# Kernel optimization log

Hardware: AMD Instinct MI355X
Metric: run time of the kernel (lower is better)

Reference implementation:

```python
import jax, jax.numpy as jnp
import numpy as np

GRID = 14    # grid_size[0]
PATCH = 16   # patch_size[0]

def setup_inputs() -> dict:
    key = jax.random.key(0)
    x = jax.random.normal(key, (32, 96, 224, 224), dtype=jnp.float32)
    return {"x": x}

def reference(x):
    # x: [B, C, H, W] with H = W = GRID*PATCH
    B, C, H, W = x.shape
    g, p = GRID, PATCH
    # [B, C, gi, pi, gj, pj]
    t = x.reshape(B, C, g, p, g, p)
    # L2 norm over (C, gi, gj) for each intra-patch offset (pi, pj) -> [B, p, p]
    sq = jnp.sum(t * t, axis=(1, 2, 4))
    norms = jnp.sqrt(sq)
    # argmax over flattened (pi, pj), pj fastest -> matches torch reshape order
    idx = jnp.argmax(norms.reshape(B, p * p), axis=1)
    si = idx // p  # row shift
    sj = idx % p   # col shift
    # circular pad + translate-by-(si,sj) + crop == circular roll by (-si, -sj)
    out = jax.vmap(lambda xi, a, b: jnp.roll(xi, (-a, -b), axis=(1, 2)))(x, si, sj)
    return out
```

## Files before the change

### kernel.cpp

```cpp
#include <hip/hip_runtime.h>

#define H 224
#define W 224
#define B 32
#define C 96


__global__ void zero_norms_kernel(float* __restrict__ nbuf) {
    int i = blockIdx.x * blockDim.x + threadIdx.x;
    nbuf[i] = 0.0f;
}

template<int DIRECT>
__global__ void norms_kernel(const float* __restrict__ x, float* __restrict__ nbuf) {
    int pi    = blockIdx.x >> 2;
    int slice = blockIdx.x & 3;
    int b     = blockIdx.y;
    int wave  = threadIdx.x >> 6;
    int lane  = threadIdx.x & 63;

    __shared__ float bins[16];
    if (threadIdx.x < 16) bins[threadIdx.x] = 0.0f;
    __syncthreads();

    if (lane < 56) {
        const float* base = x + (size_t)b * C * H * W;
        int c  = slice * 24;
        int gi = wave;
        float a0=0.f,a1=0.f,a2=0.f,a3=0.f;
        float b0=0.f,b1=0.f,b2=0.f,b3=0.f;
        #pragma unroll 2
        for (int it = 0; it < 42; ++it) {
            const float4* rowA = (const float4*)(base + ((size_t)c * H + gi * 16 + pi) * W);
            const float4* rowB = rowA + (size_t)12 * H * W / 4;
            float4 va = rowA[lane];
            float4 vb = rowB[lane];
            a0 += va.x * va.x; a1 += va.y * va.y; a2 += va.z * va.z; a3 += va.w * va.w;
            b0 += vb.x * vb.x; b1 += vb.y * vb.y; b2 += vb.z * vb.z; b3 += vb.w * vb.w;
            gi += 4; if (gi >= 14) { gi -= 14; c += 1; }
        }
        a0 += b0; a1 += b1; a2 += b2; a3 += b3;
        int bse = (lane & 3) << 2;
        atomicAdd(&bins[bse + 0], a0);
        atomicAdd(&bins[bse + 1], a1);
        atomicAdd(&bins[bse + 2], a2);
        atomicAdd(&bins[bse + 3], a3);
    }
    __syncthreads();
    if (threadIdx.x < 16) {
        if (DIRECT)
            nbuf[((slice * B + b) * 16 + pi) * 16 + threadIdx.x] = bins[threadIdx.x];
        else
            atomicAdd(&nbuf[(b * 16 + pi) * 16 + threadIdx.x], bins[threadIdx.x]);
    }
}

template<int DIRECT>
__global__ void argmax_kernel(const float* __restrict__ nbuf, int2* __restrict__ shifts) {
    int b = blockIdx.x;
    int t = threadIdx.x;
    float v = -1.0f;
    int idx = 0;
    for (int r = 0; r < 4; ++r) {
        int i = r * 64 + t;
        float u;
        if (DIRECT) {
            int o = b * 256 + i;
            u = nbuf[o] + nbuf[8192 + o] + nbuf[16384 + o] + nbuf[24576 + o];
        } else {
            u = nbuf[b * 256 + i];
        }
        if (u > v) { v = u; idx = i; }
    }
    for (int off = 32; off > 0; off >>= 1) {
        float ov = __shfl_down(v, off);
        int   oi = __shfl_down(idx, off);
        if (ov > v || (ov == v && oi < idx)) { v = ov; idx = oi; }
    }
    if (t == 0) shifts[b] = make_int2(idx >> 4, idx & 15);
}

template<int R>
__device__ __forceinline__ void roll_body(const float* __restrict__ xb,
                                          float* __restrict__ ob,
                                          int c0, int h0, int sh0,
                                          int q, int lane) {
    int v = lane + q;  if (v >= 56) v -= 56;
    int nl = lane + 1; if (nl >= 56) nl = 0;
    int sh = sh0;
    #pragma unroll
    for (int it = 0; it < 8; ++it) {
        int h = h0 + it * 4;
        const float4* srow = (const float4*)(xb + ((size_t)c0 * H + sh) * W);
        float4*       drow = (float4*)      (ob + ((size_t)c0 * H + h)  * W);
        float4 a = srow[v];
        float4 o;
        if (R == 0) {
            o = a;
        } else {
            float nx = __shfl(a.x, nl);
            float ny = (R >= 2) ? __shfl(a.y, nl) : 0.0f;
            float nz = (R == 3) ? __shfl(a.z, nl) : 0.0f;
            if (R == 1) { o.x = a.y; o.y = a.z; o.z = a.w; o.w = nx; }
            if (R == 2) { o.x = a.z; o.y = a.w; o.z = nx;  o.w = ny; }
            if (R == 3) { o.x = a.w; o.y = nx;  o.z = ny;  o.w = nz; }
        }
        drow[lane] = o;
        sh += 4; if (sh >= H) sh -= H;
    }
}

__global__ void roll_kernel(const float* __restrict__ x, float* __restrict__ out,
                            const int2* __restrict__ shifts) {
    int b     = blockIdx.y;
    int chunk = blockIdx.x;
    int wave  = threadIdx.x >> 6;
    int lane  = threadIdx.x & 63;
    if (lane >= 56) return;

    int2 s = shifts[b];
    int si = s.x, sj = s.y;
    int q = sj >> 2, r = sj & 3;

    int c0 = chunk / 7;
    int h0 = (chunk % 7) * 32 + wave;
    int sh0 = h0 + si; if (sh0 >= H) sh0 -= H;

    const float* xb = x   + (size_t)b * C * H * W;
    float*       ob = out + (size_t)b * C * H * W;

    switch (r) {
        case 0: roll_body<0>(xb, ob, c0, h0, sh0, q, lane); break;
        case 1: roll_body<1>(xb, ob, c0, h0, sh0, q, lane); break;
        case 2: roll_body<2>(xb, ob, c0, h0, sh0, q, lane); break;
        default: roll_body<3>(xb, ob, c0, h0, sh0, q, lane); break;
    }
}

extern "C" void kernel_launch(void* const* d_in, const int* in_sizes, int n_in,
                              void* d_out, int out_size, void* d_ws, size_t ws_size,
                              hipStream_t stream) {
    const float* x = (const float*)d_in[0];
    float* outp = (float*)d_out;

    const size_t directBytes = (size_t)4 * B * 256 * sizeof(float);
    if (ws_size >= directBytes + 256) {
        float* nbuf  = (float*)d_ws;
        int2* shifts = (int2*)((char*)d_ws + directBytes);
        norms_kernel<1><<<dim3(64, 32), 256, 0, stream>>>(x, nbuf);
        argmax_kernel<1><<<32, 64, 0, stream>>>(nbuf, shifts);
        roll_kernel<<<dim3(672, 32), 256, 0, stream>>>(x, outp, shifts);
    } else {
        float* nbuf  = (float*)d_ws;
        int2* shifts = (int2*)((char*)d_ws + 8192 * sizeof(float));
        zero_norms_kernel<<<32, 256, 0, stream>>>(nbuf);
        norms_kernel<0><<<dim3(64, 32), 256, 0, stream>>>(x, nbuf);
        argmax_kernel<0><<<32, 64, 0, stream>>>(nbuf, shifts);
        roll_kernel<<<dim3(672, 32), 256, 0, stream>>>(x, outp, shifts);
    }
}
```

Baseline: 353.2 us.

## Pipeline norms and roll across batch groups in a single fused kernel

Replaces the separate norms, argmax and roll kernels with one fused kernel launched in 17 stages. Each launch computes norms for batch group i and rolls batch group i-1, with the argmax folded into every roll block. The goal is to overlap the reduction pass of one group with the copy pass of the previous group, and to drop the standalone argmax launch. The cost is 17 smaller launches, plus every roll block redoing the argmax reduction. It also assumes the workspace always holds the 4-slice norm buffer and drops the small-workspace fallback.

```diff
diff --git a/kernel.cpp b/kernel.cpp
--- a/kernel.cpp
+++ b/kernel.cpp
@@ -6,79 +6,6 @@
 #define C 96
 
 
-__global__ void zero_norms_kernel(float* __restrict__ nbuf) {
-    int i = blockIdx.x * blockDim.x + threadIdx.x;
-    nbuf[i] = 0.0f;
-}
-
-template<int DIRECT>
-__global__ void norms_kernel(const float* __restrict__ x, float* __restrict__ nbuf) {
-    int pi    = blockIdx.x >> 2;
-    int slice = blockIdx.x & 3;
-    int b     = blockIdx.y;
-    int wave  = threadIdx.x >> 6;
-    int lane  = threadIdx.x & 63;
-
-    __shared__ float bins[16];
-    if (threadIdx.x < 16) bins[threadIdx.x] = 0.0f;
-    __syncthreads();
-
-    if (lane < 56) {
-        const float* base = x + (size_t)b * C * H * W;
-        int c  = slice * 24;
-        int gi = wave;
-        float a0=0.f,a1=0.f,a2=0.f,a3=0.f;
-        float b0=0.f,b1=0.f,b2=0.f,b3=0.f;
-        #pragma unroll 2
-        for (int it = 0; it < 42; ++it) {
-            const float4* rowA = (const float4*)(base + ((size_t)c * H + gi * 16 + pi) * W);
-            const float4* rowB = rowA + (size_t)12 * H * W / 4;
-            float4 va = rowA[lane];
-            float4 vb = rowB[lane];
-            a0 += va.x * va.x; a1 += va.y * va.y; a2 += va.z * va.z; a3 += va.w * va.w;
-            b0 += vb.x * vb.x; b1 += vb.y * vb.y; b2 += vb.z * vb.z; b3 += vb.w * vb.w;
-            gi += 4; if (gi >= 14) { gi -= 14; c += 1; }
-        }
-        a0 += b0; a1 += b1; a2 += b2; a3 += b3;
-        int bse = (lane & 3) << 2;
-        atomicAdd(&bins[bse + 0], a0);
-        atomicAdd(&bins[bse + 1], a1);
-        atomicAdd(&bins[bse + 2], a2);
-        atomicAdd(&bins[bse + 3], a3);
-    }
-    __syncthreads();
-    if (threadIdx.x < 16) {
-        if (DIRECT)
-            nbuf[((slice * B + b) * 16 + pi) * 16 + threadIdx.x] = bins[threadIdx.x];
-        else
-            atomicAdd(&nbuf[(b * 16 + pi) * 16 + threadIdx.x], bins[threadIdx.x]);
-    }
-}
-
-template<int DIRECT>
-__global__ void argmax_kernel(const float* __restrict__ nbuf, int2* __restrict__ shifts) {
-    int b = blockIdx.x;
-    int t = threadIdx.x;
-    float v = -1.0f;
-    int idx = 0;
-    for (int r = 0; r < 4; ++r) {
-        int i = r * 64 + t;
-        float u;
-        if (DIRECT) {
-            int o = b * 256 + i;
-            u = nbuf[o] + nbuf[8192 + o] + nbuf[16384 + o] + nbuf[24576 + o];
-        } else {
-            u = nbuf[b * 256 + i];
-        }
-        if (u > v) { v = u; idx = i; }
-    }
-    for (int off = 32; off > 0; off >>= 1) {
-        float ov = __shfl_down(v, off);
-        int   oi = __shfl_down(idx, off);
-        if (ov > v || (ov == v && oi < idx)) { v = ov; idx = oi; }
-    }
-    if (t == 0) shifts[b] = make_int2(idx >> 4, idx & 15);
-}
 
 template<int R>
 __device__ __forceinline__ void roll_body(const float* __restrict__ xb,
@@ -110,30 +37,91 @@
     }
 }
 
-__global__ void roll_kernel(const float* __restrict__ x, float* __restrict__ out,
-                            const int2* __restrict__ shifts) {
-    int b     = blockIdx.y;
-    int chunk = blockIdx.x;
-    int wave  = threadIdx.x >> 6;
-    int lane  = threadIdx.x & 63;
-    if (lane >= 56) return;
+__global__ void fused_kernel(const float* __restrict__ x, float* __restrict__ out,
+                             float* __restrict__ nbuf,
+                             int nStart, int nCount, int rStart, int rCount) {
+    int wave = threadIdx.x >> 6;
+    int lane = threadIdx.x & 63;
 
-    int2 s = shifts[b];
-    int si = s.x, sj = s.y;
-    int q = sj >> 2, r = sj & 3;
+    if ((int)blockIdx.x < nCount * 64) {
+        int b     = nStart + ((int)blockIdx.x >> 6);
+        int sub   = blockIdx.x & 63;
+        int pi    = sub >> 2;
+        int slice = sub & 3;
 
-    int c0 = chunk / 7;
-    int h0 = (chunk % 7) * 32 + wave;
-    int sh0 = h0 + si; if (sh0 >= H) sh0 -= H;
+        __shared__ float bins[16];
+        if (threadIdx.x < 16) bins[threadIdx.x] = 0.0f;
+        __syncthreads();
 
-    const float* xb = x   + (size_t)b * C * H * W;
-    float*       ob = out + (size_t)b * C * H * W;
+        if (lane < 56) {
+            const float* base = x + (size_t)b * C * H * W;
+            int c  = slice * 24;
+            int gi = wave;
+            float a0=0.f,a1=0.f,a2=0.f,a3=0.f;
+            float b0=0.f,b1=0.f,b2=0.f,b3=0.f;
+            #pragma unroll 2
+            for (int it = 0; it < 42; ++it) {
+                const float4* rowA = (const float4*)(base + ((size_t)c * H + gi * 16 + pi) * W);
+                const float4* rowB = rowA + (size_t)12 * H * W / 4;
+                float4 va = rowA[lane];
+                float4 vb = rowB[lane];
+                a0 += va.x * va.x; a1 += va.y * va.y; a2 += va.z * va.z; a3 += va.w * va.w;
+                b0 += vb.x * vb.x; b1 += vb.y * vb.y; b2 += vb.z * vb.z; b3 += vb.w * vb.w;
+                gi += 4; if (gi >= 14) { gi -= 14; c += 1; }
+            }
+            a0 += b0; a1 += b1; a2 += b2; a3 += b3;
+            int bse = (lane & 3) << 2;
+            atomicAdd(&bins[bse + 0], a0);
+            atomicAdd(&bins[bse + 1], a1);
+            atomicAdd(&bins[bse + 2], a2);
+            atomicAdd(&bins[bse + 3], a3);
+        }
+        __syncthreads();
+        if (threadIdx.x < 16)
+            nbuf[((b * 4 + slice) * 16 + pi) * 16 + threadIdx.x] = bins[threadIdx.x];
+    } else {
+        int rIdx  = blockIdx.x - nCount * 64;
+        int b     = rStart + rIdx / 672;
+        int local = rIdx % 672;
 
-    switch (r) {
-        case 0: roll_body<0>(xb, ob, c0, h0, sh0, q, lane); break;
-        case 1: roll_body<1>(xb, ob, c0, h0, sh0, q, lane); break;
-        case 2: roll_body<2>(xb, ob, c0, h0, sh0, q, lane); break;
-        default: roll_body<3>(xb, ob, c0, h0, sh0, q, lane); break;
+        const float* nb = nbuf + (size_t)b * 1024;
+        int t = threadIdx.x;
+        float v = nb[t] + nb[256 + t] + nb[512 + t] + nb[768 + t];
+        int idx = t;
+        for (int off = 32; off > 0; off >>= 1) {
+            float ov = __shfl_down(v, off);
+            int   oi = __shfl_down(idx, off);
+            if (ov > v || (ov == v && oi < idx)) { v = ov; idx = oi; }
+        }
+        __shared__ float wv[4];
+        __shared__ int   wi[4];
+        __shared__ int   ssi, ssj;
+        if (lane == 0) { wv[wave] = v; wi[wave] = idx; }
+        __syncthreads();
+        if (threadIdx.x == 0) {
+            float bv = wv[0]; int bi = wi[0];
+            #pragma unroll
+            for (int w = 1; w < 4; ++w)
+                if (wv[w] > bv) { bv = wv[w]; bi = wi[w]; }
+            ssi = bi >> 4; ssj = bi & 15;
+        }
+        __syncthreads();
+        int si = ssi, sj = ssj;
+
+        if (lane < 56) {
+            int q = sj >> 2, r = sj & 3;
+            int c0 = local / 7;
+            int h0 = (local % 7) * 32 + wave;
+            int sh0 = h0 + si; if (sh0 >= H) sh0 -= H;
+            const float* xb = x   + (size_t)b * C * H * W;
+            float*       ob = out + (size_t)b * C * H * W;
+            switch (r) {
+                case 0: roll_body<0>(xb, ob, c0, h0, sh0, q, lane); break;
+                case 1: roll_body<1>(xb, ob, c0, h0, sh0, q, lane); break;
+                case 2: roll_body<2>(xb, ob, c0, h0, sh0, q, lane); break;
+                default: roll_body<3>(xb, ob, c0, h0, sh0, q, lane); break;
+            }
+        }
     }
 }
 
@@ -142,20 +130,17 @@
                               hipStream_t stream) {
     const float* x = (const float*)d_in[0];
     float* outp = (float*)d_out;
+    float* nbuf = (float*)d_ws;
 
-    const size_t directBytes = (size_t)4 * B * 256 * sizeof(float);
-    if (ws_size >= directBytes + 256) {
-        float* nbuf  = (float*)d_ws;
-        int2* shifts = (int2*)((char*)d_ws + directBytes);
-        norms_kernel<1><<<dim3(64, 32), 256, 0, stream>>>(x, nbuf);
-        argmax_kernel<1><<<32, 64, 0, stream>>>(nbuf, shifts);
-        roll_kernel<<<dim3(672, 32), 256, 0, stream>>>(x, outp, shifts);
-    } else {
-        float* nbuf  = (float*)d_ws;
-        int2* shifts = (int2*)((char*)d_ws + 8192 * sizeof(float));
-        zero_norms_kernel<<<32, 256, 0, stream>>>(nbuf);
-        norms_kernel<0><<<dim3(64, 32), 256, 0, stream>>>(x, nbuf);
-        argmax_kernel<0><<<32, 64, 0, stream>>>(nbuf, shifts);
-        roll_kernel<<<dim3(672, 32), 256, 0, stream>>>(x, outp, shifts);
+    const int GROUP = 2;
+    const int NSTAGE = B / GROUP;
+    for (int i = 0; i <= NSTAGE; ++i) {
+        int nStart = GROUP * i;
+        int nCount = (i < NSTAGE) ? GROUP : 0;
+        int rStart = GROUP * (i - 1);
+        int rCount = (i > 0) ? GROUP : 0;
+        int blocks = nCount * 64 + rCount * 672;
+        fused_kernel<<<blocks, 256, 0, stream>>>(x, outp, nbuf,
+                                                 nStart, nCount, rStart, rCount);
     }
 }
```

After: 476.1 us. 1.35x slower.
